# Kernel tuning notes

Measured on AMD Instinct MI355X. Metric: run time of the kernel, lower is better.

The kernel has to match this reference:

```python
import jax, jax.numpy as jnp
import numpy as np

B, C, T_TEXT, T_FEAT = 16, 256, 512, 4096
DELTA = 0.1  # temperature


def setup_inputs() -> dict:
    key = jax.random.key(0)
    k1, k2 = jax.random.split(key)
    x = jax.random.normal(k1, (B, C, T_TEXT), dtype=jnp.float32)
    # durations: avg ~8 frames per token so cumsum spans ~T_FEAT frames
    w = jax.random.uniform(k2, (B, T_TEXT), dtype=jnp.float32) * 16.0
    x_mask = jnp.ones((B, T_FEAT), dtype=bool)   # frame-level mask (B, T_feat)
    y_mask = jnp.ones((B, T_TEXT), dtype=bool)   # token-level mask (B, T_text)
    return {"x": x, "w": w, "x_mask": x_mask, "y_mask": y_mask}


def reference(x, w, x_mask, y_mask):
    # x: (B, C, T_text), w: (B, T_text)
    t_feat = x_mask.shape[-1]
    # frame time grid, masked frames zeroed as in reference impl
    t = jnp.arange(t_feat, dtype=x.dtype)[None, :] * x_mask.astype(x.dtype)  # (B, T_feat)
    # Gaussian centers per token: cumulative duration minus half of own duration
    c = jnp.cumsum(w, axis=-1) - 0.5 * w  # (B, T_text)
    # energy: -delta * (t - c)^2  -> (B, T_feat, T_text)
    energy = -DELTA * jnp.square(t[:, :, None] - c[:, None, :])
    energy = jnp.where(y_mask[:, None, :], energy, -jnp.inf)
    attn = jax.nn.softmax(energy, axis=-1)  # softmax over tokens (T_text)
    # weighted sum over tokens: (B, T_feat, T_text) x (B, C, T_text) -> (B, C, T_feat)
    return jnp.einsum('bft,bct->bcf', attn, x)
```

## Files before the change

kernel.cpp:

```cpp
#include <hip/hip_runtime.h>
#include <math.h>


constexpr int BB  = 16;
constexpr int CC  = 256;
constexpr int TT  = 512;
constexpr int TF  = 4096;
constexpr float DEL = 0.1f;

constexpr int TILE_F = 32;
constexpr int NCG    = 8;
constexpr int CPT    = CC / NCG;
constexpr int MAXW   = 32;
constexpr float CUT  = 200.0f;

__global__ __launch_bounds__(256)
void centers_k(const float* __restrict__ w, float* __restrict__ cw) {
  __shared__ double dA[TT];
  __shared__ double dB[TT];
  const int b = blockIdx.x, tid = threadIdx.x;
  const float* wr = w + b * TT;
  const float w0 = wr[tid];
  const float w1 = wr[tid + 256];
  dA[tid]       = (double)w0;
  dA[tid + 256] = (double)w1;
  __syncthreads();
  double* src = dA;
  double* dst = dB;
  for (int off = 1; off < TT; off <<= 1) {
    double v0 = src[tid]       + (tid       >= off ? src[tid - off]       : 0.0);
    double v1 = src[tid + 256] + (tid + 256 >= off ? src[tid + 256 - off] : 0.0);
    dst[tid] = v0; dst[tid + 256] = v1;
    __syncthreads();
    double* t = src; src = dst; dst = t;
  }
  cw[b * TT + tid]       = (float)(src[tid]       - 0.5 * (double)w0);
  cw[b * TT + tid + 256] = (float)(src[tid + 256] - 0.5 * (double)w1);
}

__global__ __launch_bounds__(256, 4)
void gauss_up(const float* __restrict__ x, const float* __restrict__ cw,
              float* __restrict__ out) {
  __shared__ float sc[TT];
  __shared__ float pbuf[TILE_F][MAXW + 1];
  __shared__ int   s_lo[TILE_F];
  __shared__ int   s_n[TILE_F];

  const int b   = blockIdx.y;
  const int f0  = blockIdx.x * TILE_F;
  const int tid = threadIdx.x;

  sc[tid]       = cw[b * TT + tid];
  sc[tid + 256] = cw[b * TT + tid + 256];
  __syncthreads();

  if (tid < TILE_F) {
    const float fv = (float)(f0 + tid);
    int l = 0, h = TT;
    while (l < h) { int m = (l + h) >> 1; if (sc[m] < fv) l = m + 1; else h = m; }
    int jstar = (l < TT) ? l : TT - 1;
    float dmin = fabsf(sc[jstar] - fv);
    if (l > 0) { float d = fabsf(sc[l - 1] - fv); if (d <= dmin) { dmin = d; jstar = l - 1; } }
    const float D = sqrtf(fmaf(dmin, dmin, CUT));
    int lo = 0; h = TT;
    { const float lv = fv - D;
      while (lo < h) { int m = (lo + h) >> 1; if (sc[m] < lv) lo = m + 1; else h = m; } }
    int hi = lo; h = TT;
    { const float hv = fv + D;
      while (hi < h) { int m = (hi + h) >> 1; if (sc[m] <= hv) hi = m + 1; else h = m; } }
    if (hi - lo > MAXW) {
      int nl = jstar - MAXW / 2; if (nl < lo) nl = lo;
      lo = nl;
      if (hi > lo + MAXW) hi = lo + MAXW;
    }
    const int n = hi - lo;
    const float m0 = DEL * dmin * dmin;
    float Z = 0.f;
    for (int j = 0; j < n; ++j) {
      const float d = fv - sc[lo + j];
      const float e = __expf(fmaf(-DEL, d * d, m0));
      pbuf[tid][j] = e;
      Z += e;
    }
    const float rz = 1.f / Z;
    for (int j = 0; j < n; ++j) pbuf[tid][j] *= rz;
    s_lo[tid] = lo;
    s_n[tid]  = n;
  }
  __syncthreads();

  const int fi = tid & (TILE_F - 1);
  const int cg = tid / TILE_F;
  const int lo = s_lo[fi];
  const int n  = s_n[fi];

  const float* xr = x + ((size_t)b * CC + (size_t)cg * CPT) * TT + lo;
  float acc[CPT];
#pragma unroll
  for (int k = 0; k < CPT; ++k) acc[k] = 0.f;

  for (int j = 0; j < n; ++j) {
    const float p = pbuf[fi][j];
#pragma unroll
    for (int k = 0; k < CPT; ++k)
      acc[k] = fmaf(p, xr[(size_t)k * TT + j], acc[k]);
  }

  float* orow = out + ((size_t)b * CC + (size_t)cg * CPT) * TF + (f0 + fi);
#pragma unroll
  for (int k = 0; k < CPT; ++k)
    __builtin_nontemporal_store(acc[k], orow + (size_t)k * TF);
}

extern "C" void kernel_launch(void* const* d_in, const int* in_sizes, int n_in,
                              void* d_out, int out_size, void* d_ws, size_t ws_size,
                              hipStream_t stream) {
  const float* x = (const float*)d_in[0];
  const float* w = (const float*)d_in[1];
  float* out = (float*)d_out;
  float* cw  = (float*)d_ws;

  centers_k<<<dim3(BB), dim3(256), 0, stream>>>(w, cw);
  gauss_up<<<dim3(TF / TILE_F, BB), dim3(256), 0, stream>>>(x, cw, out);
}
```

Measured before the change: 106.3 us.

## Restructure upsampling to per-channel threads with shared tile token window

Each thread of the main kernel now owns one channel and accumulates all 32 frames of the tile. The 32 frames share a common, 4-aligned token window stored transposed in shared memory and zero-padded, so x is read once per channel as float4 and the output is written with float4 stores. Previously each thread handled one frame and 32 channels with strided scalar x loads and scalar nontemporal stores. The prefix-sum kernel is also rewritten as a single-wavefront shuffle scan. The shared window is capped at 64 tokens, which changes how contributions are truncated if frame windows diverge, and the 32 accumulators raise register pressure.

```diff
diff --git a/kernel.cpp b/kernel.cpp
--- a/kernel.cpp
+++ b/kernel.cpp
@@ -9,42 +9,37 @@
 constexpr float DEL = 0.1f;
 
 constexpr int TILE_F = 32;
-constexpr int NCG    = 8;
-constexpr int CPT    = CC / NCG;
 constexpr int MAXW   = 32;
+constexpr int MAXN   = 64;
 constexpr float CUT  = 200.0f;
 
-__global__ __launch_bounds__(256)
+__global__ __launch_bounds__(64)
 void centers_k(const float* __restrict__ w, float* __restrict__ cw) {
-  __shared__ double dA[TT];
-  __shared__ double dB[TT];
-  const int b = blockIdx.x, tid = threadIdx.x;
-  const float* wr = w + b * TT;
-  const float w0 = wr[tid];
-  const float w1 = wr[tid + 256];
-  dA[tid]       = (double)w0;
-  dA[tid + 256] = (double)w1;
-  __syncthreads();
-  double* src = dA;
-  double* dst = dB;
-  for (int off = 1; off < TT; off <<= 1) {
-    double v0 = src[tid]       + (tid       >= off ? src[tid - off]       : 0.0);
-    double v1 = src[tid + 256] + (tid + 256 >= off ? src[tid + 256 - off] : 0.0);
-    dst[tid] = v0; dst[tid + 256] = v1;
-    __syncthreads();
-    double* t = src; src = dst; dst = t;
+  const int b = blockIdx.x, l = threadIdx.x;
+  const float* wr = w + b * TT + l * 8;
+  float v[8];
+  *(float4*)&v[0] = *(const float4*)&wr[0];
+  *(float4*)&v[4] = *(const float4*)&wr[4];
+  double s[8]; double run = 0.0;
+#pragma unroll
+  for (int k = 0; k < 8; ++k) { run += (double)v[k]; s[k] = run; }
+  double tot = run;
+  for (int off = 1; off < 64; off <<= 1) {
+    double o = __shfl_up(tot, off, 64);
+    if (l >= off) tot += o;
   }
-  cw[b * TT + tid]       = (float)(src[tid]       - 0.5 * (double)w0);
-  cw[b * TT + tid + 256] = (float)(src[tid + 256] - 0.5 * (double)w1);
+  const double base = tot - run;
+  float* co = cw + b * TT + l * 8;
+#pragma unroll
+  for (int k = 0; k < 8; ++k) co[k] = (float)(base + s[k] - 0.5 * (double)v[k]);
 }
 
 __global__ __launch_bounds__(256, 4)
 void gauss_up(const float* __restrict__ x, const float* __restrict__ cw,
               float* __restrict__ out) {
   __shared__ float sc[TT];
-  __shared__ float pbuf[TILE_F][MAXW + 1];
-  __shared__ int   s_lo[TILE_F];
-  __shared__ int   s_n[TILE_F];
+  __shared__ __align__(16) float pbuf[MAXN][TILE_F];
+  __shared__ int s_info[2];
 
   const int b   = blockIdx.y;
   const int f0  = blockIdx.x * TILE_F;
@@ -52,6 +47,9 @@
 
   sc[tid]       = cw[b * TT + tid];
   sc[tid + 256] = cw[b * TT + tid + 256];
+#pragma unroll
+  for (int k = 0; k < MAXN * TILE_F / 256; ++k)
+    ((float*)pbuf)[tid + 256 * k] = 0.f;
   __syncthreads();
 
   if (tid < TILE_F) {
@@ -73,43 +71,74 @@
       lo = nl;
       if (hi > lo + MAXW) hi = lo + MAXW;
     }
-    const int n = hi - lo;
+
+    int LO = lo, HI = hi;
+#pragma unroll
+    for (int m = 16; m >= 1; m >>= 1) {
+      LO = min(LO, __shfl_xor(LO, m, 32));
+      HI = max(HI, __shfl_xor(HI, m, 32));
+    }
+    int LO4 = LO & ~3;
+    if (HI - LO4 > MAXN) {
+      const int js0  = __shfl(jstar, 0, 32);
+      const int js31 = __shfl(jstar, 31, 32);
+      int nl = (((js0 + js31) >> 1) - MAXN / 2) & ~3;
+      if (nl < LO4) nl = LO4;
+      LO4 = nl;
+      if (HI > LO4 + MAXN) HI = LO4 + MAXN;
+      if (lo < LO4) lo = LO4;
+      if (hi > HI)  hi = HI;
+      if (lo >= hi) {
+        lo = min(max(jstar, LO4), HI - 1); hi = lo + 1;
+      }
+    }
+
+    const int n_f = hi - lo;
+    const int j0  = lo - LO4;
     const float m0 = DEL * dmin * dmin;
     float Z = 0.f;
-    for (int j = 0; j < n; ++j) {
+    for (int j = 0; j < n_f; ++j) {
       const float d = fv - sc[lo + j];
       const float e = __expf(fmaf(-DEL, d * d, m0));
-      pbuf[tid][j] = e;
+      pbuf[j0 + j][tid] = e;
       Z += e;
     }
     const float rz = 1.f / Z;
-    for (int j = 0; j < n; ++j) pbuf[tid][j] *= rz;
-    s_lo[tid] = lo;
-    s_n[tid]  = n;
+    for (int j = 0; j < n_f; ++j) pbuf[j0 + j][tid] *= rz;
+    if (tid == 0) { s_info[0] = LO4; s_info[1] = (HI - LO4 + 3) >> 2; }
   }
   __syncthreads();
 
-  const int fi = tid & (TILE_F - 1);
-  const int cg = tid / TILE_F;
-  const int lo = s_lo[fi];
-  const int n  = s_n[fi];
+  const int LO4 = s_info[0];
+  const int NC  = s_info[1];
+  const float* xr = x + ((size_t)b * CC + tid) * TT + LO4;
 
-  const float* xr = x + ((size_t)b * CC + (size_t)cg * CPT) * TT + lo;
-  float acc[CPT];
+  float acc[TILE_F];
 #pragma unroll
-  for (int k = 0; k < CPT; ++k) acc[k] = 0.f;
+  for (int k = 0; k < TILE_F; ++k) acc[k] = 0.f;
 
-  for (int j = 0; j < n; ++j) {
-    const float p = pbuf[fi][j];
+  for (int jc = 0; jc < NC; ++jc) {
+    const float4 xv = *(const float4*)(xr + 4 * jc);
 #pragma unroll
-    for (int k = 0; k < CPT; ++k)
-      acc[k] = fmaf(p, xr[(size_t)k * TT + j], acc[k]);
+    for (int jj = 0; jj < 4; ++jj) {
+      const float xs = ((const float*)&xv)[jj];
+      const float4* prow = (const float4*)&pbuf[4 * jc + jj][0];
+#pragma unroll
+      for (int g = 0; g < TILE_F / 4; ++g) {
+        const float4 pv = prow[g];
+        acc[4 * g + 0] = fmaf(pv.x, xs, acc[4 * g + 0]);
+        acc[4 * g + 1] = fmaf(pv.y, xs, acc[4 * g + 1]);
+        acc[4 * g + 2] = fmaf(pv.z, xs, acc[4 * g + 2]);
+        acc[4 * g + 3] = fmaf(pv.w, xs, acc[4 * g + 3]);
+      }
+    }
   }
 
-  float* orow = out + ((size_t)b * CC + (size_t)cg * CPT) * TF + (f0 + fi);
+  float* orow = out + ((size_t)b * CC + tid) * TF + f0;
 #pragma unroll
-  for (int k = 0; k < CPT; ++k)
-    __builtin_nontemporal_store(acc[k], orow + (size_t)k * TF);
+  for (int g = 0; g < TILE_F / 4; ++g)
+    *(float4*)(orow + 4 * g) =
+        make_float4(acc[4 * g], acc[4 * g + 1], acc[4 * g + 2], acc[4 * g + 3]);
 }
 
 extern "C" void kernel_launch(void* const* d_in, const int* in_sizes, int n_in,
@@ -120,6 +149,6 @@
   float* out = (float*)d_out;
   float* cw  = (float*)d_ws;
 
-  centers_k<<<dim3(BB), dim3(256), 0, stream>>>(w, cw);
+  centers_k<<<dim3(BB), dim3(64), 0, stream>>>(w, cw);
   gauss_up<<<dim3(TF / TILE_F, BB), dim3(256), 0, stream>>>(x, cw, out);
 }
```

After: 116.1 us. 9.2% more time.
